# Optimization experiments

Measured on AMD Instinct MI355X. Metric: run time of the kernel, lower is better.

Reference implementation:

```python
import jax, jax.numpy as jnp
import numpy as np

B, C, H, W = 8, 256, 64, 64
HEADS = 8
DH = C // HEADS          # dim_head = in_ch // heads (as constructed in BasicTransBlock)
RS = 16                  # reduce_size
EPS = 1e-5               # BatchNorm eps


def _rel_pos_index():
    # Swin-style relative position index over the RS x RS reduced grid
    coords = np.stack(np.meshgrid(np.arange(RS), np.arange(RS), indexing='ij')).reshape(2, -1)
    rel = coords[:, :, None] - coords[:, None, :]
    rel = rel.transpose(1, 2, 0).copy()
    rel[:, :, 0] += RS - 1
    rel[:, :, 1] += RS - 1
    rel[:, :, 0] *= 2 * RS - 1
    return jnp.asarray(rel.sum(-1))  # [RS*RS, RS*RS] int

REL_IDX = _rel_pos_index()


def setup_inputs() -> dict:
    key = jax.random.key(0)
    ks = jax.random.split(key, 8)
    f32 = jnp.float32
    return {
        "x": jax.random.normal(ks[0], (B, C, H, W), f32),
        "bn1_gamma": jnp.ones((C,), f32),
        "bn1_beta": jnp.zeros((C,), f32),
        "bn1_mean": jnp.zeros((C,), f32),
        "bn1_var": jnp.ones((C,), f32),
        "qkv_dw": jax.random.normal(ks[1], (C, 1, 3, 3), f32) * 0.05,   # depthwise 3x3
        "qkv_pw": jax.random.normal(ks[2], (3 * C, C), f32) * 0.05,     # pointwise 1x1 -> 3C
        "out_dw": jax.random.normal(ks[3], (C, 1, 3, 3), f32) * 0.05,
        "out_pw": jax.random.normal(ks[4], (C, C), f32) * 0.05,
        "rel_table": jax.random.normal(ks[5], ((2 * RS - 1) ** 2, HEADS), f32) * 0.02,
        "bn2_gamma": jnp.ones((C,), f32),
        "bn2_beta": jnp.zeros((C,), f32),
        "bn2_mean": jnp.zeros((C,), f32),
        "bn2_var": jnp.ones((C,), f32),
        "mlp_w": jax.random.normal(ks[6], (C, C), f32) * 0.05,          # 1x1 conv, no bias
    }


def _bn(x, gamma, beta, mean, var):
    # inference-mode BatchNorm2d
    inv = gamma * jax.lax.rsqrt(var + EPS)
    return x * inv[None, :, None, None] + (beta - mean * inv)[None, :, None, None]


def _dwconv3(x, w):
    # depthwise 3x3, stride 1, padding 1
    return jax.lax.conv_general_dilated(
        x, w, (1, 1), 'SAME', feature_group_count=x.shape[1],
        dimension_numbers=('NCHW', 'OIHW', 'NCHW'))


def _interp_ac(x, oh, ow):
    # bilinear resize, align_corners=True (matches F.interpolate(..., align_corners=True))
    _, _, h, w = x.shape
    ys = jnp.linspace(0.0, h - 1.0, oh)
    xs = jnp.linspace(0.0, w - 1.0, ow)
    y0 = jnp.floor(ys).astype(jnp.int32); y1 = jnp.minimum(y0 + 1, h - 1)
    x0 = jnp.floor(xs).astype(jnp.int32); x1 = jnp.minimum(x0 + 1, w - 1)
    wy = (ys - y0.astype(ys.dtype))[:, None]   # [oh,1]
    wx = (xs - x0.astype(xs.dtype))            # [ow]
    v = x[:, :, y0, :] * (1 - wy) + x[:, :, y1, :] * wy      # [B,C,oh,w]
    return v[:, :, :, x0] * (1 - wx) + v[:, :, :, x1] * wx   # [B,C,oh,ow]


def _split_heads(t, h, w):
    # channel layout in rearrange is (dim_head heads): c = d*HEADS + head
    b = t.shape[0]
    return t.reshape(b, DH, HEADS, h * w).transpose(0, 2, 3, 1)  # [B,heads,hw,DH]


def _rel_bias(rel_table):
    bias = rel_table[REL_IDX.reshape(-1)].reshape(RS, RS, RS * RS, HEADS)
    bias = jnp.repeat(bias, H // RS, axis=0)   # expand rows to H
    bias = jnp.repeat(bias, W // RS, axis=1)   # expand cols to W
    return bias.reshape(H * W, RS * RS, HEADS).transpose(2, 0, 1)  # [heads, HW, RS*RS]


def reference(x, bn1_gamma, bn1_beta, bn1_mean, bn1_var,
              qkv_dw, qkv_pw, out_dw, out_pw, rel_table,
              bn2_gamma, bn2_beta, bn2_mean, bn2_var, mlp_w):
    out = _bn(x, bn1_gamma, bn1_beta, bn1_mean, bn1_var)

    # --- LinearAttention ---
    qkv = jnp.einsum('bchw,oc->bohw', _dwconv3(out, qkv_dw), qkv_pw)
    q, k, v = jnp.split(qkv, 3, axis=1)
    k = _interp_ac(k, RS, RS)
    v = _interp_ac(v, RS, RS)
    q = _split_heads(q, H, W)       # [B,heads,HW,DH]
    k = _split_heads(k, RS, RS)     # [B,heads,RS^2,DH]
    v = _split_heads(v, RS, RS)
    attn = jnp.einsum('bhid,bhjd->bhij', q, k)
    attn = (attn + _rel_bias(rel_table)[None]) * (DH ** -0.5)  # bias added BEFORE scale, as in source
    attn = jax.nn.softmax(attn, axis=-1)
    o = jnp.einsum('bhij,bhjd->bhid', attn, v)                 # [B,heads,HW,DH]
    o = o.transpose(0, 3, 1, 2).reshape(x.shape[0], C, H, W)   # inverse of (dim_head heads) split
    o = jnp.einsum('bchw,oc->bohw', _dwconv3(o, out_dw), out_pw)

    out = o + x
    residue = out
    out = jax.nn.relu(_bn(out, bn2_gamma, bn2_beta, bn2_mean, bn2_var))
    out = jnp.einsum('bchw,oc->bohw', out, mlp_w)
    return out + residue
```

## Files before the change

kernel.cpp:

```cpp
#include <hip/hip_runtime.h>
#include <hip/hip_bf16.h>
#include <math.h>

#define EPSF 1e-5f

typedef float f32x4 __attribute__((ext_vector_type(4)));
typedef short short8 __attribute__((ext_vector_type(8)));
typedef short short4v __attribute__((ext_vector_type(4)));
typedef unsigned short u16x4 __attribute__((ext_vector_type(4)));

static __device__ __forceinline__ unsigned short f2bf(float f) {
    unsigned u = __float_as_uint(f);
    u = (u + 0x7FFF + ((u >> 16) & 1)) >> 16;
    return (unsigned short)u;
}

static __device__ __forceinline__ float bf2f(unsigned short u) {
    return __uint_as_float((unsigned)u << 16);
}

static __device__ __forceinline__ unsigned packbf2(float a, float b) {
    __hip_bfloat162 t = __float22bfloat162_rn(float2{a, b});
    union { __hip_bfloat162 v; unsigned u; } cv;
    cv.v = t;
    return cv.u;
}

static __device__ __forceinline__ int swz(int r) { return ((r ^ (r >> 2)) & 7) << 1; }

template<bool BN, bool IB, bool OBF>
__global__ __launch_bounds__(256) void dwconv_k(
    const void* __restrict__ X, const float* __restrict__ DW,
    const float* __restrict__ g, const float* __restrict__ be,
    const float* __restrict__ mn, const float* __restrict__ vr,
    void* __restrict__ Out)
{
    int tid = threadIdx.x;
    int plane = blockIdx.x * 2 + (tid >> 7);
    int c = plane & 255;
    float inv = 1.f, ad = 0.f;
    if (BN) {
        inv = g[c] * rsqrtf(vr[c] + EPSF);
        ad  = be[c] - mn[c] * inv;
    }
    float w[9];
#pragma unroll
    for (int i = 0; i < 9; ++i) w[i] = DW[c * 9 + i];
    const float* Xf          = (const float*)X + (size_t)plane * 4096;
    const unsigned short* Xh = (const unsigned short*)X + (size_t)plane * 4096;
    int u  = tid & 127;
    int y0 = (u >> 3) * 4;
    int x0 = (u & 7) * 8;

    float r[6][16];
#pragma unroll
    for (int rr = 0; rr < 6; ++rr) {
        int yy = y0 + rr - 1;
        bool rv = (unsigned)yy < 64u;
#pragma unroll
        for (int gq = 0; gq < 4; ++gq) {
            int xx = x0 - 4 + gq * 4;
            f32x4 v = {0.f, 0.f, 0.f, 0.f};
            if (rv && (unsigned)xx < 64u) {
                if (IB) {
                    u16x4 u4 = *(const u16x4*)&Xh[yy * 64 + xx];
                    v[0] = bf2f(u4[0]); v[1] = bf2f(u4[1]);
                    v[2] = bf2f(u4[2]); v[3] = bf2f(u4[3]);
                } else {
                    v = *(const f32x4*)&Xf[yy * 64 + xx];
                }
                if (BN) {
#pragma unroll
                    for (int j = 0; j < 4; ++j) v[j] = v[j] * inv + ad;
                }
            }
            r[rr][gq * 4 + 0] = v[0]; r[rr][gq * 4 + 1] = v[1];
            r[rr][gq * 4 + 2] = v[2]; r[rr][gq * 4 + 3] = v[3];
        }
    }

#pragma unroll
    for (int j = 0; j < 4; ++j) {
        float acc[8] = {};
#pragma unroll
        for (int ky = 0; ky < 3; ++ky) {
#pragma unroll
            for (int kx = 0; kx < 3; ++kx) {
                float ww = w[ky * 3 + kx];
#pragma unroll
                for (int p = 0; p < 8; ++p)
                    acc[p] += ww * r[j + ky][3 + p + kx];
            }
        }
        if (OBF) {
            unsigned short* Ob = (unsigned short*)Out + (size_t)plane * 4096;
            int4 pk = { (int)packbf2(acc[0], acc[1]), (int)packbf2(acc[2], acc[3]),
                        (int)packbf2(acc[4], acc[5]), (int)packbf2(acc[6], acc[7]) };
            *(int4*)&Ob[(y0 + j) * 64 + x0] = pk;
        } else {
            float* Ob = (float*)Out + (size_t)plane * 4096;
            f32x4 lo = {acc[0], acc[1], acc[2], acc[3]};
            f32x4 hi = {acc[4], acc[5], acc[6], acc[7]};
            *(f32x4*)&Ob[(y0 + j) * 64 + x0]     = lo;
            *(f32x4*)&Ob[(y0 + j) * 64 + x0 + 4] = hi;
        }
    }
}

__global__ __launch_bounds__(256) void interp_k(
    const unsigned short* __restrict__ T, float* __restrict__ R)
{
    int bc = blockIdx.x;
    const unsigned short* Tb = T + (size_t)bc * 4096;
    int p  = threadIdx.x;
    int oy = p >> 4, ox = p & 15;
    const float st = 63.0f / 15.0f;
    float fy = oy * st, fx = ox * st;
    int y0 = (int)floorf(fy); int y1 = min(y0 + 1, 63); float wy = fy - (float)y0;
    int x0 = (int)floorf(fx); int x1 = min(x0 + 1, 63); float wx = fx - (float)x0;
    float v00 = bf2f(Tb[y0 * 64 + x0]), v01 = bf2f(Tb[y0 * 64 + x1]);
    float v10 = bf2f(Tb[y1 * 64 + x0]), v11 = bf2f(Tb[y1 * 64 + x1]);
    R[(size_t)bc * 256 + p] =
        (1.f - wy) * ((1.f - wx) * v00 + wx * v01) +
        wy         * ((1.f - wx) * v10 + wx * v11);
}

__global__ __launch_bounds__(256) void bias_k(
    const float* __restrict__ rel, float* __restrict__ btab)
{
    int idx = blockIdx.x * 256 + threadIdx.x;
    int h   = idx >> 16;
    int qc  = (idx >> 8) & 255;
    int key = idx & 255;
    int ay = qc >> 4, ax = qc & 15, by = key >> 4, bx = key & 15;
    int t = (ay - by + 15) * 31 + (ax - bx + 15);
    btab[idx] = rel[t * 8 + h];
}

__global__ __launch_bounds__(256) void kvt_k(
    const unsigned short* __restrict__ kv,
    unsigned short* __restrict__ khat, unsigned short* __restrict__ vhat)
{
    __shared__ unsigned short kt_[32 * 260];
    int bh = blockIdx.x;
    int b = bh >> 3, h = bh & 7;
    const unsigned short* kvb = kv + (size_t)b * 512 * 256;
    int tid = threadIdx.x;

#pragma unroll
    for (int it = 0; it < 8; ++it) {
        int idx = it * 256 + tid;
        int d = idx >> 6, k4 = (idx & 63) * 4;
        ushort4 v = *(const ushort4*)&kvb[(size_t)(256 + d * 8 + h) * 256 + k4];
        *(ushort4*)&vhat[(size_t)bh * 8192 + d * 256 + k4] = v;
    }
#pragma unroll
    for (int it = 0; it < 8; ++it) {
        int idx = it * 256 + tid;
        int d = idx >> 6, k4 = (idx & 63) * 4;
        ushort4 v = *(const ushort4*)&kvb[(size_t)(d * 8 + h) * 256 + k4];
        *(ushort4*)&kt_[d * 260 + k4] = v;
    }
    __syncthreads();
#pragma unroll
    for (int it = 0; it < 8; ++it) {
        int idx = it * 256 + tid;
        int key = idx >> 3, dq = idx & 7;
        ushort4 o;
        o.x = kt_[(dq * 4 + 0) * 260 + key];
        o.y = kt_[(dq * 4 + 1) * 260 + key];
        o.z = kt_[(dq * 4 + 2) * 260 + key];
        o.w = kt_[(dq * 4 + 3) * 260 + key];
        *(ushort4*)&khat[(size_t)bh * 8192 + key * 32 + dq * 4] = o;
    }
}

template<int MODE, bool OB, bool AB>
__global__ __launch_bounds__(256) void mgemm_k(
    const void* __restrict__ A, const float* __restrict__ W,
    float* __restrict__ Out, const float* __restrict__ X,
    const float* __restrict__ g, const float* __restrict__ be,
    const float* __restrict__ mn, const float* __restrict__ vr,
    int M, int Ntot)
{
    __shared__ short Ws[128 * 256];
    __shared__ short As[128 * 64];
    int b = blockIdx.z, m0 = blockIdx.x * 128, n0 = blockIdx.y * 128;
    int tid = threadIdx.x;
    const float* Abf          = (const float*)A + (size_t)b * 256 * M;
    const unsigned short* Abh = (const unsigned short*)A + (size_t)b * 256 * M;

#pragma unroll
    for (int it = 0; it < 32; ++it) {
        int idx = it * 256 + tid;
        int n = idx >> 6, kq = idx & 63;
        f32x4 w4 = *(const f32x4*)&W[(size_t)(n0 + n) * 256 + kq * 4];
        short4v pk = { (short)f2bf(w4[0]), (short)f2bf(w4[1]),
                       (short)f2bf(w4[2]), (short)f2bf(w4[3]) };
        *(short4v*)&Ws[n * 256 + ((kq ^ swz(n)) << 2)] = pk;
    }

    int mg = tid & 31, kg = tid >> 5;
    f32x4 rg[8];
    u16x4 rg16[8];
    auto load_tile = [&](int k0) {
#pragma unroll
        for (int half = 0; half < 2; ++half) {
#pragma unroll
            for (int i = 0; i < 4; ++i) {
                int c = k0 + kg * 4 + half * 32 + i;
                if (AB) {
                    rg16[half * 4 + i] = *(const u16x4*)&Abh[(size_t)c * M + m0 + mg * 4];
                } else {
                    f32x4 v = *(const f32x4*)&Abf[(size_t)c * M + m0 + mg * 4];
                    if (MODE == 2) {
                        float iv = g[c] * rsqrtf(vr[c] + EPSF);
                        float ad = be[c] - mn[c] * iv;
#pragma unroll
                        for (int j = 0; j < 4; ++j) v[j] = fmaxf(v[j] * iv + ad, 0.f);
                    }
                    rg[half * 4 + i] = v;
                }
            }
        }
    };
    load_tile(0);

    int w = tid >> 6, lane = tid & 63;
    int wm = w & 1, wn = w >> 1;
    int lg = lane >> 4, lc = lane & 15;
    f32x4 acc[4][4] = {};

    for (int k0 = 0; k0 < 256; k0 += 64) {
        __syncthreads();
#pragma unroll
        for (int half = 0; half < 2; ++half) {
#pragma unroll
            for (int j = 0; j < 4; ++j) {
                int m = mg * 4 + j;
                short4v pk;
                if (AB) {
                    pk = short4v{ (short)rg16[half * 4 + 0][j], (short)rg16[half * 4 + 1][j],
                                  (short)rg16[half * 4 + 2][j], (short)rg16[half * 4 + 3][j] };
                } else {
                    pk = short4v{ (short)f2bf(rg[half * 4 + 0][j]), (short)f2bf(rg[half * 4 + 1][j]),
                                  (short)f2bf(rg[half * 4 + 2][j]), (short)f2bf(rg[half * 4 + 3][j]) };
                }
                *(short4v*)&As[m * 64 + (((kg + half * 8) ^ swz(m)) << 2)] = pk;
            }
        }
        __syncthreads();
        if (k0 < 192) load_tile(k0 + 64);
#pragma unroll
        for (int ksl = 0; ksl < 2; ++ksl) {
            short8 wf[4], af[4];
            int gk = (k0 + ksl * 32 + lg * 8) >> 2;
            int ga = (ksl * 32 + lg * 8) >> 2;
#pragma unroll
            for (int nt = 0; nt < 4; ++nt) {
                int n = wn * 64 + nt * 16 + lc;
                wf[nt] = *(const short8*)&Ws[n * 256 + ((gk ^ swz(n)) << 2)];
            }
#pragma unroll
            for (int mt = 0; mt < 4; ++mt) {
                int m = wm * 64 + mt * 16 + lc;
                af[mt] = *(const short8*)&As[m * 64 + ((ga ^ swz(m)) << 2)];
            }
#pragma unroll
            for (int nt = 0; nt < 4; ++nt)
#pragma unroll
                for (int mt = 0; mt < 4; ++mt)
                    acc[nt][mt] = __builtin_amdgcn_mfma_f32_16x16x32_bf16(
                        wf[nt], af[mt], acc[nt][mt], 0, 0, 0);
        }
    }

    size_t ob = (size_t)b * Ntot * M;
#pragma unroll
    for (int nt = 0; nt < 4; ++nt) {
#pragma unroll
        for (int mt = 0; mt < 4; ++mt) {
#pragma unroll
            for (int reg = 0; reg < 4; ++reg) {
                int n = n0 + wn * 64 + nt * 16 + lg * 4 + reg;
                int m = m0 + wm * 64 + mt * 16 + lc;
                size_t addr = ob + (size_t)n * M + m;
                float v = acc[nt][mt][reg];
                if (MODE >= 1) v += X[addr];
                if (OB) ((unsigned short*)Out)[addr] = f2bf(v);
                else    Out[addr] = v;
            }
        }
    }
}

__global__ __launch_bounds__(256) void attn_mfma_k(
    const unsigned short* __restrict__ Q, const unsigned short* __restrict__ Khat,
    const unsigned short* __restrict__ Vhat,
    const float* __restrict__ btab, unsigned short* __restrict__ O)
{
    __shared__ float Om[4][16][36];
    __shared__ float Mw[4][16];
    __shared__ float Lw[4][16];

    int b = blockIdx.z, h = blockIdx.y, chunk = blockIdx.x;
    int tid = threadIdx.x;
    int w = tid >> 6, lane = tid & 63;
    int lg = lane >> 4, lc = lane & 15;
    int kw = w * 64;

    const unsigned short* Kb = Khat + (size_t)(b * 8 + h) * 8192;
    const unsigned short* Vb = Vhat + (size_t)(b * 8 + h) * 8192;
    const unsigned short* Qb = Q + (size_t)b * 256 * 4096;
    unsigned short* Ob = O + (size_t)b * 256 * 4096;
    const float* bt = btab + (size_t)h * 65536;
    int rw = chunk * 64;

    const float SCALE = 0.17677669529663687f;
    int s1 = ((lg & 1) << 5) + lc;
    int s2 = s1 + 16;
    bool useOdd = (lg >> 1) != 0;
    int mrow = tid & 15, md = tid >> 4;

    for (int mt = 0; mt < 4; ++mt) {
        int rbase = rw + mt * 16;
        int r_a = rbase + lc;
        int qc = ((r_a >> 8) << 4) | ((r_a >> 2) & 15);
        const float* bq = bt + (size_t)qc * 256 + kw + lg * 4;

        f32x4 sacc[4];
#pragma unroll
        for (int kt = 0; kt < 4; ++kt)
            sacc[kt] = *(const f32x4*)&bq[kt * 16];

        short8 qf;
#pragma unroll
        for (int j = 0; j < 8; ++j)
            qf[j] = (short)Qb[(size_t)((lg * 8 + j) * 8 + h) * 4096 + r_a];

#pragma unroll
        for (int kt = 0; kt < 4; ++kt) {
            short8 kf = *(const short8*)&Kb[(kw + kt * 16 + lc) * 32 + lg * 8];
            sacc[kt] = __builtin_amdgcn_mfma_f32_16x16x32_bf16(kf, qf, sacc[kt], 0, 0, 0);
        }

        float mx = -1e30f;
#pragma unroll
        for (int kt = 0; kt < 4; ++kt)
            mx = fmaxf(mx, fmaxf(fmaxf(sacc[kt][0], sacc[kt][1]),
                                 fmaxf(sacc[kt][2], sacc[kt][3])));
        mx = fmaxf(mx, __shfl_xor(mx, 16));
        mx = fmaxf(mx, __shfl_xor(mx, 32));
        float nms = -mx * SCALE;

        float ls = 0.f;
        unsigned plo[4], phi[4];
#pragma unroll
        for (int kt = 0; kt < 4; ++kt) {
            float p0 = __expf(fmaf(sacc[kt][0], SCALE, nms));
            float p1 = __expf(fmaf(sacc[kt][1], SCALE, nms));
            float p2 = __expf(fmaf(sacc[kt][2], SCALE, nms));
            float p3 = __expf(fmaf(sacc[kt][3], SCALE, nms));
            ls += (p0 + p1) + (p2 + p3);
            plo[kt] = packbf2(p0, p1);
            phi[kt] = packbf2(p2, p3);
        }
        ls += __shfl_xor(ls, 16);
        ls += __shfl_xor(ls, 32);

        f32x4 o0 = {0.f, 0.f, 0.f, 0.f}, o1 = {0.f, 0.f, 0.f, 0.f};
#pragma unroll
        for (int ks = 0; ks < 2; ++ks) {
            int eA = __shfl((int)plo[2 * ks], s1), oA = __shfl((int)plo[2 * ks + 1], s1);
            int eB = __shfl((int)phi[2 * ks], s1), oB = __shfl((int)phi[2 * ks + 1], s1);
            int eC = __shfl((int)plo[2 * ks], s2), oC = __shfl((int)plo[2 * ks + 1], s2);
            int eD = __shfl((int)phi[2 * ks], s2), oD = __shfl((int)phi[2 * ks + 1], s2);
            int4 pi = { useOdd ? oA : eA, useOdd ? oB : eB,
                        useOdd ? oC : eC, useOdd ? oD : eD };
            short8 pf = *(short8*)&pi;
            short8 v0 = *(const short8*)&Vb[lc * 256 + kw + ks * 32 + lg * 8];
            short8 v1 = *(const short8*)&Vb[(16 + lc) * 256 + kw + ks * 32 + lg * 8];
            o0 = __builtin_amdgcn_mfma_f32_16x16x32_bf16(v0, pf, o0, 0, 0, 0);
            o1 = __builtin_amdgcn_mfma_f32_16x16x32_bf16(v1, pf, o1, 0, 0, 0);
        }

        *(f32x4*)&Om[w][lc][lg * 4]      = o0;
        *(f32x4*)&Om[w][lc][16 + lg * 4] = o1;
        if (lg == 0) { Mw[w][lc] = mx; Lw[w][lc] = ls; }
        __syncthreads();

        {
            float m0 = Mw[0][mrow], m1 = Mw[1][mrow];
            float m2 = Mw[2][mrow], m3 = Mw[3][mrow];
            float M = fmaxf(fmaxf(m0, m1), fmaxf(m2, m3));
            float e0 = __expf((m0 - M) * SCALE);
            float e1 = __expf((m1 - M) * SCALE);
            float e2 = __expf((m2 - M) * SCALE);
            float e3 = __expf((m3 - M) * SCALE);
            float L = Lw[0][mrow] * e0 + Lw[1][mrow] * e1
                    + Lw[2][mrow] * e2 + Lw[3][mrow] * e3;
            float inv = 1.f / L;
            float a0 = Om[0][mrow][md] * e0 + Om[1][mrow][md] * e1
                     + Om[2][mrow][md] * e2 + Om[3][mrow][md] * e3;
            float a1 = Om[0][mrow][md + 16] * e0 + Om[1][mrow][md + 16] * e1
                     + Om[2][mrow][md + 16] * e2 + Om[3][mrow][md + 16] * e3;
            Ob[(size_t)(md * 8 + h) * 4096 + rbase + mrow]        = f2bf(a0 * inv);
            Ob[(size_t)((md + 16) * 8 + h) * 4096 + rbase + mrow] = f2bf(a1 * inv);
        }
        __syncthreads();
    }
}

extern "C" void kernel_launch(void* const* d_in, const int* in_sizes, int n_in,
                              void* d_out, int out_size, void* d_ws, size_t ws_size,
                              hipStream_t stream)
{
    const float* x       = (const float*)d_in[0];
    const float* bn1_g   = (const float*)d_in[1];
    const float* bn1_b   = (const float*)d_in[2];
    const float* bn1_m   = (const float*)d_in[3];
    const float* bn1_v   = (const float*)d_in[4];
    const float* qkv_dw  = (const float*)d_in[5];
    const float* qkv_pw  = (const float*)d_in[6];
    const float* out_dw  = (const float*)d_in[7];
    const float* out_pw  = (const float*)d_in[8];
    const float* rel     = (const float*)d_in[9];
    const float* bn2_g   = (const float*)d_in[10];
    const float* bn2_b   = (const float*)d_in[11];
    const float* bn2_m   = (const float*)d_in[12];
    const float* bn2_v   = (const float*)d_in[13];
    const float* mlp_w   = (const float*)d_in[14];
    float* out = (float*)d_out;

    float* ws = (float*)d_ws;
    float* t    = ws;
    float* q    = ws + (size_t)8 * 1024 * 1024;
    float* tr   = ws + (size_t)16 * 1024 * 1024;
    float* kv   = tr + 524288;
    float* btab = kv + 524288;
    float* khat = btab + 524288;
    float* vhat = khat + 262144;
    float* o   = t;
    float* t2  = q;
    float* a   = t;

    bias_k<<<dim3(2048), 256, 0, stream>>>(rel, btab);

    dwconv_k<true, false, true><<<dim3(1024), 256, 0, stream>>>(
        x, qkv_dw, bn1_g, bn1_b, bn1_m, bn1_v, t);

    mgemm_k<0, true, true><<<dim3(32, 2, 8), 256, 0, stream>>>(
        t, qkv_pw, q, nullptr, nullptr, nullptr, nullptr, nullptr,
        4096, 256);

    interp_k<<<dim3(2048), 256, 0, stream>>>((const unsigned short*)t, tr);

    mgemm_k<0, true, false><<<dim3(2, 4, 8), 256, 0, stream>>>(
        tr, qkv_pw + 256 * 256, kv, nullptr, nullptr, nullptr, nullptr, nullptr,
        256, 512);

    kvt_k<<<dim3(64), 256, 0, stream>>>(
        (const unsigned short*)kv, (unsigned short*)khat, (unsigned short*)vhat);

    attn_mfma_k<<<dim3(64, 8, 8), 256, 0, stream>>>(
        (const unsigned short*)q, (const unsigned short*)khat,
        (const unsigned short*)vhat, btab, (unsigned short*)o);

    dwconv_k<false, true, true><<<dim3(1024), 256, 0, stream>>>(
        o, out_dw, nullptr, nullptr, nullptr, nullptr, t2);

    mgemm_k<1, false, true><<<dim3(32, 2, 8), 256, 0, stream>>>(
        t2, out_pw, a, x, nullptr, nullptr, nullptr, nullptr,
        4096, 256);

    mgemm_k<2, false, false><<<dim3(32, 2, 8), 256, 0, stream>>>(
        a, mlp_w, out, a, bn2_g, bn2_b, bn2_m, bn2_v,
        4096, 256);
}
```

Before: 137.2 us.

## Double-buffer attention merge, hoist K/V fragments, double rows per block

The attention kernel now loads the K and V MFMA fragments into registers once per block instead of once per 16-row tile. The score/softmax/PV step for the next tile runs before the cross-wave merge of the current tile, using double-buffered shared memory, which removes one barrier per tile. Each block now covers 128 query rows, so the grid is halved to 2048 blocks. This cuts redundant K/V loads and barrier stalls, at the cost of more registers and LDS per block and fewer blocks to fill the GPU.

```diff
diff --git a/kernel.cpp b/kernel.cpp
--- a/kernel.cpp
+++ b/kernel.cpp
@@ -299,9 +299,9 @@
     const unsigned short* __restrict__ Vhat,
     const float* __restrict__ btab, unsigned short* __restrict__ O)
 {
-    __shared__ float Om[4][16][36];
-    __shared__ float Mw[4][16];
-    __shared__ float Lw[4][16];
+    __shared__ float Om[2][4][16][36];
+    __shared__ float Mw[2][4][16];
+    __shared__ float Lw[2][4][16];
 
     int b = blockIdx.z, h = blockIdx.y, chunk = blockIdx.x;
     int tid = threadIdx.x;
@@ -314,7 +314,7 @@
     const unsigned short* Qb = Q + (size_t)b * 256 * 4096;
     unsigned short* Ob = O + (size_t)b * 256 * 4096;
     const float* bt = btab + (size_t)h * 65536;
-    int rw = chunk * 64;
+    int rw = chunk * 128;
 
     const float SCALE = 0.17677669529663687f;
     int s1 = ((lg & 1) << 5) + lc;
@@ -322,7 +322,17 @@
     bool useOdd = (lg >> 1) != 0;
     int mrow = tid & 15, md = tid >> 4;
 
-    for (int mt = 0; mt < 4; ++mt) {
+    short8 kf[4], vf0[2], vf1[2];
+#pragma unroll
+    for (int kt = 0; kt < 4; ++kt)
+        kf[kt] = *(const short8*)&Kb[(kw + kt * 16 + lc) * 32 + lg * 8];
+#pragma unroll
+    for (int ks = 0; ks < 2; ++ks) {
+        vf0[ks] = *(const short8*)&Vb[lc * 256 + kw + ks * 32 + lg * 8];
+        vf1[ks] = *(const short8*)&Vb[(16 + lc) * 256 + kw + ks * 32 + lg * 8];
+    }
+
+    auto compute = [&](int mt, int buf) {
         int rbase = rw + mt * 16;
         int r_a = rbase + lc;
         int qc = ((r_a >> 8) << 4) | ((r_a >> 2) & 15);
@@ -339,10 +349,8 @@
             qf[j] = (short)Qb[(size_t)((lg * 8 + j) * 8 + h) * 4096 + r_a];
 
 #pragma unroll
-        for (int kt = 0; kt < 4; ++kt) {
-            short8 kf = *(const short8*)&Kb[(kw + kt * 16 + lc) * 32 + lg * 8];
-            sacc[kt] = __builtin_amdgcn_mfma_f32_16x16x32_bf16(kf, qf, sacc[kt], 0, 0, 0);
-        }
+        for (int kt = 0; kt < 4; ++kt)
+            sacc[kt] = __builtin_amdgcn_mfma_f32_16x16x32_bf16(kf[kt], qf, sacc[kt], 0, 0, 0);
 
         float mx = -1e30f;
 #pragma unroll
@@ -378,36 +386,40 @@
             int4 pi = { useOdd ? oA : eA, useOdd ? oB : eB,
                         useOdd ? oC : eC, useOdd ? oD : eD };
             short8 pf = *(short8*)&pi;
-            short8 v0 = *(const short8*)&Vb[lc * 256 + kw + ks * 32 + lg * 8];
-            short8 v1 = *(const short8*)&Vb[(16 + lc) * 256 + kw + ks * 32 + lg * 8];
-            o0 = __builtin_amdgcn_mfma_f32_16x16x32_bf16(v0, pf, o0, 0, 0, 0);
-            o1 = __builtin_amdgcn_mfma_f32_16x16x32_bf16(v1, pf, o1, 0, 0, 0);
-        }
-
-        *(f32x4*)&Om[w][lc][lg * 4]      = o0;
-        *(f32x4*)&Om[w][lc][16 + lg * 4] = o1;
-        if (lg == 0) { Mw[w][lc] = mx; Lw[w][lc] = ls; }
+            o0 = __builtin_amdgcn_mfma_f32_16x16x32_bf16(vf0[ks], pf, o0, 0, 0, 0);
+            o1 = __builtin_amdgcn_mfma_f32_16x16x32_bf16(vf1[ks], pf, o1, 0, 0, 0);
+        }
+
+        *(f32x4*)&Om[buf][w][lc][lg * 4]      = o0;
+        *(f32x4*)&Om[buf][w][lc][16 + lg * 4] = o1;
+        if (lg == 0) { Mw[buf][w][lc] = mx; Lw[buf][w][lc] = ls; }
+    };
+
+    auto merge = [&](int mt, int buf) {
+        int rbase = rw + mt * 16;
+        float m0 = Mw[buf][0][mrow], m1 = Mw[buf][1][mrow];
+        float m2 = Mw[buf][2][mrow], m3 = Mw[buf][3][mrow];
+        float M = fmaxf(fmaxf(m0, m1), fmaxf(m2, m3));
+        float e0 = __expf((m0 - M) * SCALE);
+        float e1 = __expf((m1 - M) * SCALE);
+        float e2 = __expf((m2 - M) * SCALE);
+        float e3 = __expf((m3 - M) * SCALE);
+        float L = Lw[buf][0][mrow] * e0 + Lw[buf][1][mrow] * e1
+                + Lw[buf][2][mrow] * e2 + Lw[buf][3][mrow] * e3;
+        float inv = 1.f / L;
+        float a0 = Om[buf][0][mrow][md] * e0 + Om[buf][1][mrow][md] * e1
+                 + Om[buf][2][mrow][md] * e2 + Om[buf][3][mrow][md] * e3;
+        float a1 = Om[buf][0][mrow][md + 16] * e0 + Om[buf][1][mrow][md + 16] * e1
+                 + Om[buf][2][mrow][md + 16] * e2 + Om[buf][3][mrow][md + 16] * e3;
+        Ob[(size_t)(md * 8 + h) * 4096 + rbase + mrow]        = f2bf(a0 * inv);
+        Ob[(size_t)((md + 16) * 8 + h) * 4096 + rbase + mrow] = f2bf(a1 * inv);
+    };
+
+    compute(0, 0);
+    for (int mt = 0; mt < 8; ++mt) {
         __syncthreads();
-
-        {
-            float m0 = Mw[0][mrow], m1 = Mw[1][mrow];
-            float m2 = Mw[2][mrow], m3 = Mw[3][mrow];
-            float M = fmaxf(fmaxf(m0, m1), fmaxf(m2, m3));
-            float e0 = __expf((m0 - M) * SCALE);
-            float e1 = __expf((m1 - M) * SCALE);
-            float e2 = __expf((m2 - M) * SCALE);
-            float e3 = __expf((m3 - M) * SCALE);
-            float L = Lw[0][mrow] * e0 + Lw[1][mrow] * e1
-                    + Lw[2][mrow] * e2 + Lw[3][mrow] * e3;
-            float inv = 1.f / L;
-            float a0 = Om[0][mrow][md] * e0 + Om[1][mrow][md] * e1
-                     + Om[2][mrow][md] * e2 + Om[3][mrow][md] * e3;
-            float a1 = Om[0][mrow][md + 16] * e0 + Om[1][mrow][md + 16] * e1
-                     + Om[2][mrow][md + 16] * e2 + Om[3][mrow][md + 16] * e3;
-            Ob[(size_t)(md * 8 + h) * 4096 + rbase + mrow]        = f2bf(a0 * inv);
-            Ob[(size_t)((md + 16) * 8 + h) * 4096 + rbase + mrow] = f2bf(a1 * inv);
-        }
-        __syncthreads();
+        if (mt < 7) compute(mt + 1, (mt + 1) & 1);
+        merge(mt, mt & 1);
     }
 }
 
@@ -462,7 +474,7 @@
     kvt_k<<<dim3(64), 256, 0, stream>>>(
         (const unsigned short*)kv, (unsigned short*)khat, (unsigned short*)vhat);
 
-    attn_mfma_k<<<dim3(64, 8, 8), 256, 0, stream>>>(
+    attn_mfma_k<<<dim3(32, 8, 8), 256, 0, stream>>>(
         (const unsigned short*)q, (const unsigned short*)khat,
         (const unsigned short*)vhat, btab, (unsigned short*)o);
 
```

Measured after the change: 137.5 us. Within noise of the previous version (+0.2%).
